# Kernel optimization log

Hardware: AMD Instinct MI355X
Metric: run time of the kernel (lower is better)

The kernel has to match this reference:

```python
import jax, jax.numpy as jnp
import numpy as np

D = 1024
E = 8


def setup_inputs() -> dict:
    key = jax.random.key(0)
    ks = jax.random.split(key, 7)
    s = 1.0 / np.sqrt(D)
    x = jax.random.normal(ks[0], (4, 2048, D), dtype=jnp.float32)
    Wg = jax.random.uniform(ks[1], (D, E), minval=-s, maxval=s, dtype=jnp.float32)
    bg = jax.random.uniform(ks[2], (E,), minval=-s, maxval=s, dtype=jnp.float32)
    W1 = jax.random.uniform(ks[3], (E, D, D), minval=-s, maxval=s, dtype=jnp.float32)
    b1 = jax.random.uniform(ks[4], (E, D), minval=-s, maxval=s, dtype=jnp.float32)
    W2 = jax.random.uniform(ks[5], (E, D, D), minval=-s, maxval=s, dtype=jnp.float32)
    b2 = jax.random.uniform(ks[6], (E, D), minval=-s, maxval=s, dtype=jnp.float32)
    return {"x": x, "Wg": Wg, "bg": bg, "W1": W1, "b1": b1, "W2": W2, "b2": b2}


def reference(x, Wg, bg, W1, b1, W2, b2):
    N, T, d = x.shape
    x_flat = x.reshape(N * T, d)                                  # [NT, D]
    logits = x_flat @ Wg + bg                                     # [NT, E]
    probs = jax.nn.softmax(logits, axis=-1)
    assignments = jnp.argmax(probs, axis=-1)                      # [NT]
    # all-experts MLP (dense, as in the original module)
    h = jnp.einsum('nd,edh->neh', x_flat, W1) + b1[None]          # [NT, E, D]
    h = jax.nn.gelu(h, approximate=False)                         # torch GELU = exact erf
    eo = jnp.einsum('neh,ehd->ned', h, W2) + b2[None]             # [NT, E, D]
    selected = jnp.take_along_axis(eo, assignments[:, None, None], axis=1)[:, 0, :]  # [NT, D]
    w = jnp.take_along_axis(probs, assignments[:, None], axis=1)  # [NT, 1]
    out = (w * selected).reshape(N, T, d)
    return out
```

## Files before the change

### kernel.cpp

```cpp
#include <hip/hip_runtime.h>
#include <cstdint>

#define NT 8192
#define DD 1024
#define NE 8
#define BK 64
#define NKIT (DD / BK)
#define TM 128
#define MAXTILE 72
#define TPX (MAXTILE / 8)

typedef __attribute__((ext_vector_type(8))) _Float16 half8;
typedef __attribute__((ext_vector_type(4))) float f32x4;

__device__ __forceinline__ unsigned short f2h_bits(float f) {
  _Float16 h = (_Float16)f;
  return __builtin_bit_cast(unsigned short, h);
}

#define GLDS16(gp, lp) __builtin_amdgcn_global_load_lds( \
  (__attribute__((address_space(1))) void*)(uintptr_t)(gp), \
  (__attribute__((address_space(3))) void*)(uintptr_t)(lp), 16, 0, 0)

#define WAITCNT_VM0  0xF70

__global__ __launch_bounds__(256) void prep_kernel(
    const float* __restrict__ W1, const float* __restrict__ W2,
    _Float16* __restrict__ W1t, _Float16* __restrict__ W2t,
    const float* __restrict__ x, const float* __restrict__ Wg, const float* __restrict__ bg,
    int* __restrict__ assign, float* __restrict__ wgt, _Float16* __restrict__ xh) {
  __shared__ alignas(16) char smem[32768];
  const int bid = blockIdx.x;
  const int tid = threadIdx.x;
  if (bid < 4096) {
    float (*tile)[65] = (float (*)[65])smem;
    const int z = bid >> 8;
    const float* W = (z < 8 ? W1 : W2) + (size_t)(z & 7) * (DD * DD);
    _Float16* Wt   = (z < 8 ? W1t : W2t) + (size_t)(z & 7) * (DD * DD);
    const int k0 = (bid & 15) * 64, n0 = ((bid >> 4) & 15) * 64;
#pragma unroll
    for (int it = 0; it < 4; ++it) {
      int idx = it * 256 + tid;
      int r = idx >> 4;
      int q = idx & 15;
      float4 v = *(const float4*)(W + (size_t)(k0 + r) * DD + n0 + q * 4);
      tile[r][q * 4 + 0] = v.x; tile[r][q * 4 + 1] = v.y;
      tile[r][q * 4 + 2] = v.z; tile[r][q * 4 + 3] = v.w;
    }
    __syncthreads();
#pragma unroll
    for (int it = 0; it < 4; ++it) {
      int idx = it * 256 + tid;
      int n = idx >> 4;
      int q = idx & 15;
      ushort4 o;
      o.x = f2h_bits(tile[q * 4 + 0][n]);
      o.y = f2h_bits(tile[q * 4 + 1][n]);
      o.z = f2h_bits(tile[q * 4 + 2][n]);
      o.w = f2h_bits(tile[q * 4 + 3][n]);
      *(ushort4*)(Wt + (size_t)(n0 + n) * DD + k0 + q * 4) = o;
    }
  } else {
    float* WgL = (float*)smem;
    const int gb = bid - 4096;
#pragma unroll
    for (int it = 0; it < 8; ++it) {
      int idx = it * 256 + tid;
      float4 v = ((const float4*)Wg)[idx];
      int k = idx >> 1;
      int e0 = (idx & 1) * 4;
      WgL[(e0 + 0) * DD + k] = v.x;
      WgL[(e0 + 1) * DD + k] = v.y;
      WgL[(e0 + 2) * DD + k] = v.z;
      WgL[(e0 + 3) * DD + k] = v.w;
    }
    __syncthreads();
    const int lane = tid & 63, w = tid >> 6;
#pragma unroll
    for (int s = 0; s < 2; ++s) {
      const int t = gb * 8 + w * 2 + s;
      const float4* xr = (const float4*)(x + (size_t)t * DD);
      float4 xv[4];
#pragma unroll
      for (int c = 0; c < 4; ++c) xv[c] = xr[lane + 64 * c];
      ushort4* xo = (ushort4*)(xh + (size_t)t * DD);
#pragma unroll
      for (int c = 0; c < 4; ++c) {
        union { ushort4 u; _Float16 h[4]; } cv;
        cv.h[0] = (_Float16)xv[c].x; cv.h[1] = (_Float16)xv[c].y;
        cv.h[2] = (_Float16)xv[c].z; cv.h[3] = (_Float16)xv[c].w;
        xo[lane + 64 * c] = cv.u;
      }
      float p[NE];
#pragma unroll
      for (int e = 0; e < NE; ++e) {
        float acc = 0.f;
#pragma unroll
        for (int c = 0; c < 4; ++c) {
          float4 wv = *(const float4*)&WgL[e * DD + 4 * lane + 256 * c];
          acc += xv[c].x * wv.x + xv[c].y * wv.y + xv[c].z * wv.z + xv[c].w * wv.w;
        }
        p[e] = acc;
      }
#pragma unroll
      for (int e = 0; e < NE; ++e) {
        float v = p[e];
        for (int off = 32; off > 0; off >>= 1) v += __shfl_down(v, off, 64);
        p[e] = v;
      }
      if (lane == 0) {
        float l[NE];
#pragma unroll
        for (int e = 0; e < NE; ++e) l[e] = p[e] + bg[e];
        int a = 0; float best = l[0];
#pragma unroll
        for (int e = 1; e < NE; ++e) if (l[e] > best) { best = l[e]; a = e; }
        float sum = 0.f;
#pragma unroll
        for (int e = 0; e < NE; ++e) sum += expf(l[e] - best);
        assign[t] = a;
        wgt[t] = 1.0f / sum;
      }
    }
  }
}

__global__ __launch_bounds__(1024) void sort_kernel(
    const int* __restrict__ assign, int* __restrict__ rowtok, int* __restrict__ plan) {
  __shared__ int sc[NE * 1024];
  __shared__ int s_pref[NE + 1];
  const int tid = threadIdx.x;
  int a[8];
  int c[NE];
#pragma unroll
  for (int e = 0; e < NE; ++e) c[e] = 0;
#pragma unroll
  for (int j = 0; j < 8; ++j) { a[j] = assign[tid * 8 + j]; ++c[a[j]]; }
#pragma unroll
  for (int e = 0; e < NE; ++e) sc[e * 1024 + tid] = c[e];
  __syncthreads();
  for (int d = 1; d < 1024; d <<= 1) {
    int add[NE];
    if (tid >= d) {
#pragma unroll
      for (int e = 0; e < NE; ++e) add[e] = sc[e * 1024 + tid - d];
    }
    __syncthreads();
    if (tid >= d) {
#pragma unroll
      for (int e = 0; e < NE; ++e) sc[e * 1024 + tid] += add[e];
    }
    __syncthreads();
  }
  int tot[NE], incl[NE];
#pragma unroll
  for (int e = 0; e < NE; ++e) { tot[e] = sc[e * 1024 + 1023]; incl[e] = sc[e * 1024 + tid]; }
  int offs[NE];
  {
    int s = 0;
#pragma unroll
    for (int e = 0; e < NE; ++e) { offs[e] = s; s += tot[e]; }
  }
  int run[NE];
#pragma unroll
  for (int e = 0; e < NE; ++e) run[e] = offs[e] + incl[e] - c[e];
#pragma unroll
  for (int j = 0; j < 8; ++j) { int e = a[j]; rowtok[run[e]++] = tid * 8 + j; }
  if (tid == 0) {
    int s = 0;
    for (int e = 0; e < NE; ++e) { s_pref[e] = s; s += (tot[e] + TM - 1) / TM; }
    s_pref[NE] = s;
    plan[0] = s;
  }
  __syncthreads();
  const int nt = s_pref[NE];
  if (tid < nt) {
    int e = 0;
    while (tid >= s_pref[e + 1]) ++e;
    int t = tid - s_pref[e];
    plan[1 + tid] = e;
    plan[1 + MAXTILE + tid] = offs[e] + t * TM;
    plan[1 + 2 * MAXTILE + tid] = offs[e] + tot[e];
  }
}

template <int MODE>
__global__ __launch_bounds__(256, 2) void gemm_kernel(
    const _Float16* __restrict__ A,
    const _Float16* __restrict__ Wt,
    const float* __restrict__ bias,
    const int* __restrict__ plan,
    _Float16* __restrict__ Hout,
    float* __restrict__ Fout,
    const int* __restrict__ rowtok,
    const float* __restrict__ wgt) {
  const int wrk = blockIdx.x;
  const int g = wrk & 7;
  const int r = wrk >> 3;
  const int tile = g * TPX + (r >> 3);
  const int nb = r & 7;
  if (tile >= plan[0]) return;
  const int e = plan[1 + tile];
  const int m0 = plan[1 + MAXTILE + tile];
  const int seg_end = plan[1 + 2 * MAXTILE + tile];
  const int n0 = nb * 128;

  const int tid = threadIdx.x;
  const int lane = tid & 63;
  const int wv = tid >> 6;
  const int wm = wv >> 1;
  const int wq = wv & 1;
  const int quad = lane >> 4;
  const int r15 = lane & 15;

  __shared__ alignas(16) char lds[65536];

  const _Float16* We = Wt + (size_t)e * DD * DD;
  const _Float16* gAp[4];
  const _Float16* gBp[4];
  int ldsoA[4], ldsoB[4];
#pragma unroll
  for (int i = 0; i < 4; ++i) {
    int slot = i * 256 + tid;
    int row = slot >> 3;
    int c = (slot & 7) ^ (row & 7);
    int rg = m0 + row; if (rg > NT - 1) rg = NT - 1;
    int arow = (MODE == 0) ? rowtok[rg] : rg;
    gAp[i] = A + (size_t)arow * DD + c * 8;
    ldsoA[i] = slot * 16;
    gBp[i] = We + (size_t)(n0 + row) * DD + c * 8;
    ldsoB[i] = slot * 16;
  }

  int aoff[4][2], boff[4][2];
#pragma unroll
  for (int i = 0; i < 4; ++i) {
#pragma unroll
    for (int q = 0; q < 2; ++q) {
      int m = wm * 64 + i * 16 + r15;
      aoff[i][q] = m * 8 + ((q * 4 + quad) ^ (r15 & 7));
      int n = wq * 64 + i * 16 + r15;
      boff[i][q] = n * 8 + ((q * 4 + quad) ^ (r15 & 7));
    }
  }

  f32x4 acc[4][4];
  f32x4 zero4 = {0.f, 0.f, 0.f, 0.f};
#pragma unroll
  for (int mi = 0; mi < 4; ++mi)
#pragma unroll
    for (int ni = 0; ni < 4; ++ni) acc[mi][ni] = zero4;

#define LDSBUF(B) (lds + (B) * 32768)
#define STAGE(KT, BUF) do {                                          \
    const int ko_ = (KT) * BK;                                       \
    char* lb_ = LDSBUF(BUF);                                         \
    GLDS16(gAp[0] + ko_, lb_ + ldsoA[0]);                            \
    GLDS16(gAp[1] + ko_, lb_ + ldsoA[1]);                            \
    GLDS16(gAp[2] + ko_, lb_ + ldsoA[2]);                            \
    GLDS16(gAp[3] + ko_, lb_ + ldsoA[3]);                            \
    GLDS16(gBp[0] + ko_, lb_ + 16384 + ldsoB[0]);                    \
    GLDS16(gBp[1] + ko_, lb_ + 16384 + ldsoB[1]);                    \
    GLDS16(gBp[2] + ko_, lb_ + 16384 + ldsoB[2]);                    \
    GLDS16(gBp[3] + ko_, lb_ + 16384 + ldsoB[3]);                    \
  } while (0)
#define COMPUTE(BUF) do {                                            \
    const half8* AsV = (const half8*)(LDSBUF(BUF));                  \
    const half8* BsV = (const half8*)(LDSBUF(BUF) + 16384);          \
    _Pragma("unroll")                                                \
    for (int q = 0; q < 2; ++q) {                                    \
      half8 a_[4], b_[4];                                            \
      _Pragma("unroll")                                              \
      for (int i = 0; i < 4; ++i) a_[i] = AsV[aoff[i][q]];           \
      _Pragma("unroll")                                              \
      for (int i = 0; i < 4; ++i) b_[i] = BsV[boff[i][q]];           \
      _Pragma("unroll")                                              \
      for (int mi = 0; mi < 4; ++mi)                                 \
        _Pragma("unroll")                                            \
        for (int ni = 0; ni < 4; ++ni)                               \
          acc[mi][ni] = __builtin_amdgcn_mfma_f32_16x16x32_f16(a_[mi], b_[ni], acc[mi][ni], 0, 0, 0); \
    }                                                                \
  } while (0)

  STAGE(0, 0);
  __builtin_amdgcn_s_waitcnt(WAITCNT_VM0);
  __builtin_amdgcn_s_barrier();
  __asm__ volatile("" ::: "memory");

#pragma unroll 1
  for (int kt = 0; kt < NKIT; ++kt) {
    const int buf = kt & 1;
    if (kt + 1 < NKIT) STAGE(kt + 1, buf ^ 1);
    COMPUTE(buf);
    __builtin_amdgcn_s_waitcnt(WAITCNT_VM0);
    __builtin_amdgcn_s_barrier();
    __asm__ volatile("" ::: "memory");
  }
#undef COMPUTE
#undef STAGE
#undef LDSBUF

  const float* bptr = bias + (size_t)e * DD;
#pragma unroll
  for (int mi = 0; mi < 4; ++mi) {
    int rowb = m0 + wm * 64 + mi * 16 + quad * 4;
#pragma unroll
    for (int rr = 0; rr < 4; ++rr) {
      int gpos = rowb + rr;
      if (gpos < seg_end) {
        if (MODE == 0) {
#pragma unroll
          for (int ni = 0; ni < 4; ++ni) {
            int n = n0 + wq * 64 + ni * 16 + r15;
            float val = acc[mi][ni][rr] + bptr[n];
            val = 0.5f * val * (1.0f + erff(val * 0.70710678118654752f));
            Hout[(size_t)gpos * DD + n] = (_Float16)val;
          }
        } else {
          int tok = rowtok[gpos];
          float wgl = wgt[tok];
          float* orow = Fout + (size_t)tok * DD;
#pragma unroll
          for (int ni = 0; ni < 4; ++ni) {
            int n = n0 + wq * 64 + ni * 16 + r15;
            orow[n] = (acc[mi][ni][rr] + bptr[n]) * wgl;
          }
        }
      }
    }
  }
}

extern "C" void kernel_launch(void* const* d_in, const int* in_sizes, int n_in,
                              void* d_out, int out_size, void* d_ws, size_t ws_size,
                              hipStream_t stream) {
  const float* x  = (const float*)d_in[0];
  const float* Wg = (const float*)d_in[1];
  const float* bg = (const float*)d_in[2];
  const float* W1 = (const float*)d_in[3];
  const float* b1 = (const float*)d_in[4];
  const float* W2 = (const float*)d_in[5];
  const float* b2 = (const float*)d_in[6];
  float* out = (float*)d_out;

  char* ws = (char*)d_ws;
  const size_t MB16 = (size_t)1 << 24;
  _Float16* W1t = (_Float16*)(ws + 0 * MB16);
  _Float16* W2t = (_Float16*)(ws + 1 * MB16);
  _Float16* xh  = (_Float16*)(ws + 2 * MB16);
  _Float16* H   = (_Float16*)(ws + 3 * MB16);
  int*   assign = (int*)(ws + 4 * MB16);
  int*   rowtok = assign + NT;
  float* wgt    = (float*)(rowtok + NT);
  int*   plan   = (int*)(wgt + NT);

  prep_kernel<<<4096 + NT / 8, 256, 0, stream>>>(W1, W2, W1t, W2t, x, Wg, bg, assign, wgt, xh);
  sort_kernel<<<1, 1024, 0, stream>>>(assign, rowtok, plan);
  gemm_kernel<0><<<MAXTILE * 8, 256, 0, stream>>>(xh, W1t, b1, plan, H, nullptr, rowtok, nullptr);
  gemm_kernel<1><<<MAXTILE * 8, 256, 0, stream>>>(H, W2t, b2, plan, nullptr, out, rowtok, wgt);
}
```

Baseline: 244.5 us.

## Enlarge grouped GEMM tiles to 256x256 with 512-thread blocks

Doubles the M and N block tile of both expert GEMMs to 256x256, moves to 8 waves per block with each wave owning a 128x64 sub-tile, and doubles the double-buffered LDS to 128KB. Larger tiles raise arithmetic intensity and cut redundant global and LDS traffic for the activations and expert weights. In exchange, the grid shrinks to at most 160 blocks, fewer than the CU count. Per-thread accumulators double and LDS use likely allows one block per CU, so occupancy and load balance across partial expert tiles may suffer.

```diff
diff --git a/kernel.cpp b/kernel.cpp
--- a/kernel.cpp
+++ b/kernel.cpp
@@ -6,9 +6,10 @@
 #define NE 8
 #define BK 64
 #define NKIT (DD / BK)
-#define TM 128
-#define MAXTILE 72
+#define TM 256
+#define MAXTILE 40
 #define TPX (MAXTILE / 8)
+#define NBLK 4
 
 typedef __attribute__((ext_vector_type(8))) _Float16 half8;
 typedef __attribute__((ext_vector_type(4))) float f32x4;
@@ -185,7 +186,7 @@
 }
 
 template <int MODE>
-__global__ __launch_bounds__(256, 2) void gemm_kernel(
+__global__ __launch_bounds__(512, 2) void gemm_kernel(
     const _Float16* __restrict__ A,
     const _Float16* __restrict__ Wt,
     const float* __restrict__ bias,
@@ -197,88 +198,91 @@
   const int wrk = blockIdx.x;
   const int g = wrk & 7;
   const int r = wrk >> 3;
-  const int tile = g * TPX + (r >> 3);
-  const int nb = r & 7;
+  const int tile = g * TPX + (r >> 2);
+  const int nb = r & 3;
   if (tile >= plan[0]) return;
   const int e = plan[1 + tile];
   const int m0 = plan[1 + MAXTILE + tile];
   const int seg_end = plan[1 + 2 * MAXTILE + tile];
-  const int n0 = nb * 128;
+  const int n0 = nb * 256;
 
   const int tid = threadIdx.x;
   const int lane = tid & 63;
   const int wv = tid >> 6;
-  const int wm = wv >> 1;
-  const int wq = wv & 1;
+  const int wm = wv >> 2;
+  const int wn = wv & 3;
   const int quad = lane >> 4;
   const int r15 = lane & 15;
 
-  __shared__ alignas(16) char lds[65536];
+  __shared__ alignas(16) char lds[131072];
 
   const _Float16* We = Wt + (size_t)e * DD * DD;
   const _Float16* gAp[4];
   const _Float16* gBp[4];
-  int ldsoA[4], ldsoB[4];
+  int ldso[4];
 #pragma unroll
   for (int i = 0; i < 4; ++i) {
-    int slot = i * 256 + tid;
+    int slot = i * 512 + tid;
     int row = slot >> 3;
     int c = (slot & 7) ^ (row & 7);
     int rg = m0 + row; if (rg > NT - 1) rg = NT - 1;
     int arow = (MODE == 0) ? rowtok[rg] : rg;
     gAp[i] = A + (size_t)arow * DD + c * 8;
-    ldsoA[i] = slot * 16;
     gBp[i] = We + (size_t)(n0 + row) * DD + c * 8;
-    ldsoB[i] = slot * 16;
-  }
-
-  int aoff[4][2], boff[4][2];
-#pragma unroll
-  for (int i = 0; i < 4; ++i) {
+    ldso[i] = slot * 16;
+  }
+
+  int aoff[8][2], boff[4][2];
+#pragma unroll
+  for (int i = 0; i < 8; ++i)
 #pragma unroll
     for (int q = 0; q < 2; ++q) {
-      int m = wm * 64 + i * 16 + r15;
+      int m = wm * 128 + i * 16 + r15;
       aoff[i][q] = m * 8 + ((q * 4 + quad) ^ (r15 & 7));
-      int n = wq * 64 + i * 16 + r15;
+    }
+#pragma unroll
+  for (int i = 0; i < 4; ++i)
+#pragma unroll
+    for (int q = 0; q < 2; ++q) {
+      int n = wn * 64 + i * 16 + r15;
       boff[i][q] = n * 8 + ((q * 4 + quad) ^ (r15 & 7));
     }
-  }
-
-  f32x4 acc[4][4];
+
+  f32x4 acc[8][4];
   f32x4 zero4 = {0.f, 0.f, 0.f, 0.f};
 #pragma unroll
-  for (int mi = 0; mi < 4; ++mi)
+  for (int mi = 0; mi < 8; ++mi)
 #pragma unroll
     for (int ni = 0; ni < 4; ++ni) acc[mi][ni] = zero4;
 
-#define LDSBUF(B) (lds + (B) * 32768)
+#define LDSBUF(B) (lds + (B) * 65536)
 #define STAGE(KT, BUF) do {                                          \
     const int ko_ = (KT) * BK;                                       \
     char* lb_ = LDSBUF(BUF);                                         \
-    GLDS16(gAp[0] + ko_, lb_ + ldsoA[0]);                            \
-    GLDS16(gAp[1] + ko_, lb_ + ldsoA[1]);                            \
-    GLDS16(gAp[2] + ko_, lb_ + ldsoA[2]);                            \
-    GLDS16(gAp[3] + ko_, lb_ + ldsoA[3]);                            \
-    GLDS16(gBp[0] + ko_, lb_ + 16384 + ldsoB[0]);                    \
-    GLDS16(gBp[1] + ko_, lb_ + 16384 + ldsoB[1]);                    \
-    GLDS16(gBp[2] + ko_, lb_ + 16384 + ldsoB[2]);                    \
-    GLDS16(gBp[3] + ko_, lb_ + 16384 + ldsoB[3]);                    \
+    GLDS16(gAp[0] + ko_, lb_ + ldso[0]);                             \
+    GLDS16(gAp[1] + ko_, lb_ + ldso[1]);                             \
+    GLDS16(gAp[2] + ko_, lb_ + ldso[2]);                             \
+    GLDS16(gAp[3] + ko_, lb_ + ldso[3]);                             \
+    GLDS16(gBp[0] + ko_, lb_ + 32768 + ldso[0]);                     \
+    GLDS16(gBp[1] + ko_, lb_ + 32768 + ldso[1]);                     \
+    GLDS16(gBp[2] + ko_, lb_ + 32768 + ldso[2]);                     \
+    GLDS16(gBp[3] + ko_, lb_ + 32768 + ldso[3]);                     \
   } while (0)
 #define COMPUTE(BUF) do {                                            \
     const half8* AsV = (const half8*)(LDSBUF(BUF));                  \
-    const half8* BsV = (const half8*)(LDSBUF(BUF) + 16384);          \
+    const half8* BsV = (const half8*)(LDSBUF(BUF) + 32768);          \
     _Pragma("unroll")                                                \
     for (int q = 0; q < 2; ++q) {                                    \
-      half8 a_[4], b_[4];                                            \
-      _Pragma("unroll")                                              \
-      for (int i = 0; i < 4; ++i) a_[i] = AsV[aoff[i][q]];           \
+      half8 b_[4];                                                   \
       _Pragma("unroll")                                              \
       for (int i = 0; i < 4; ++i) b_[i] = BsV[boff[i][q]];           \
       _Pragma("unroll")                                              \
-      for (int mi = 0; mi < 4; ++mi)                                 \
+      for (int mi = 0; mi < 8; ++mi) {                               \
+        half8 a_ = AsV[aoff[mi][q]];                                 \
         _Pragma("unroll")                                            \
         for (int ni = 0; ni < 4; ++ni)                               \
-          acc[mi][ni] = __builtin_amdgcn_mfma_f32_16x16x32_f16(a_[mi], b_[ni], acc[mi][ni], 0, 0, 0); \
+          acc[mi][ni] = __builtin_amdgcn_mfma_f32_16x16x32_f16(a_, b_[ni], acc[mi][ni], 0, 0, 0); \
+      }                                                              \
     }                                                                \
   } while (0)
 
@@ -302,8 +306,8 @@
 
   const float* bptr = bias + (size_t)e * DD;
 #pragma unroll
-  for (int mi = 0; mi < 4; ++mi) {
-    int rowb = m0 + wm * 64 + mi * 16 + quad * 4;
+  for (int mi = 0; mi < 8; ++mi) {
+    int rowb = m0 + wm * 128 + mi * 16 + quad * 4;
 #pragma unroll
     for (int rr = 0; rr < 4; ++rr) {
       int gpos = rowb + rr;
@@ -311,7 +315,7 @@
         if (MODE == 0) {
 #pragma unroll
           for (int ni = 0; ni < 4; ++ni) {
-            int n = n0 + wq * 64 + ni * 16 + r15;
+            int n = n0 + wn * 64 + ni * 16 + r15;
             float val = acc[mi][ni][rr] + bptr[n];
             val = 0.5f * val * (1.0f + erff(val * 0.70710678118654752f));
             Hout[(size_t)gpos * DD + n] = (_Float16)val;
@@ -322,7 +326,7 @@
           float* orow = Fout + (size_t)tok * DD;
 #pragma unroll
           for (int ni = 0; ni < 4; ++ni) {
-            int n = n0 + wq * 64 + ni * 16 + r15;
+            int n = n0 + wn * 64 + ni * 16 + r15;
             orow[n] = (acc[mi][ni][rr] + bptr[n]) * wgl;
           }
         }
@@ -356,6 +360,6 @@
 
   prep_kernel<<<4096 + NT / 8, 256, 0, stream>>>(W1, W2, W1t, W2t, x, Wg, bg, assign, wgt, xh);
   sort_kernel<<<1, 1024, 0, stream>>>(assign, rowtok, plan);
-  gemm_kernel<0><<<MAXTILE * 8, 256, 0, stream>>>(xh, W1t, b1, plan, H, nullptr, rowtok, nullptr);
-  gemm_kernel<1><<<MAXTILE * 8, 256, 0, stream>>>(H, W2t, b2, plan, nullptr, out, rowtok, wgt);
-}
+  gemm_kernel<0><<<MAXTILE * NBLK, 512, 0, stream>>>(xh, W1t, b1, plan, H, nullptr, rowtok, nullptr);
+  gemm_kernel<1><<<MAXTILE * NBLK, 512, 0, stream>>>(H, W2t, b2, plan, nullptr, out, rowtok, wgt);
+}
```

Measured after the change: 283.1 us. 1.16x slower.
